# Kernel tuning notes

Measured on AMD Instinct MI355X. Metric: run time of the kernel, lower is better.

## Reference

```python
import jax, jax.numpy as jnp
import numpy as np

LN_EPS = 1e-5
NEG_INF = -1e30


def setup_inputs() -> dict:
    key = jax.random.key(0)
    ks = jax.random.split(key, 8)
    B, S, D_MODEL, Q_IN = 1, 2048, 1024, 512
    HI, DI = 16, 64            # indexer heads / head_dim
    H, DQK, DV = 8, 64, 64     # MLA heads, qk_head_dim, v_head_dim
    return {
        "x": jax.random.normal(ks[0], (B, S, D_MODEL), jnp.float32),
        "q_input": jax.random.normal(ks[1], (B, S, Q_IN), jnp.float32),
        "q": jax.random.normal(ks[2], (B, S, H, DQK), jnp.float32),
        "k": jax.random.normal(ks[3], (B, S, H, DQK), jnp.float32),
        "v": jax.random.normal(ks[4], (B, S, H, DV), jnp.float32),
        "w_q": jax.random.normal(ks[5], (Q_IN, HI * DI), jnp.float32) * (Q_IN ** -0.5),
        "w_k": jax.random.normal(ks[6], (D_MODEL, DI), jnp.float32) * (D_MODEL ** -0.5),
        "ln_g": jnp.ones((DI,), jnp.float32),
        "ln_b": jnp.zeros((DI,), jnp.float32),
        "w_weights": jax.random.normal(ks[7], (D_MODEL, HI), jnp.float32) * (D_MODEL ** -0.5),
        "top_k": 128,
    }


def _indexer_topk(x, q_input, w_q, w_k, ln_g, ln_b, w_weights, top_k):
    """Lightning indexer: per-head relevance scores -> weighted sum -> causal top-k indices."""
    B, S, _ = x.shape
    HI = w_weights.shape[1]
    DI = w_k.shape[1]
    qi = (q_input @ w_q).reshape(B, S, HI, DI)          # bqhd
    ki = x @ w_k                                         # bkd
    mu = ki.mean(-1, keepdims=True)
    var = ((ki - mu) ** 2).mean(-1, keepdims=True)
    ki = (ki - mu) * jax.lax.rsqrt(var + LN_EPS) * ln_g + ln_b
    # per-head weights; scores*w summed over h == (sum_h w*q) . k  (fused, same math)
    w = (x @ w_weights) * (HI ** -0.5)                   # bqh
    q_eff = jnp.einsum("bqhd,bqh->bqd", qi, w) * (DI ** -0.5)
    scores = jnp.einsum("bqd,bkd->bqk", q_eff, ki)       # [B,S,S]
    pos = jnp.arange(S)
    causal = jnp.where(pos[None, :] <= pos[:, None], 0.0, NEG_INF).astype(scores.dtype)
    scores = scores + causal[None]
    return jax.lax.top_k(scores, top_k)[1]               # [B,S,K]


def reference(x, q_input, q, k, v, w_q, w_k, ln_g, ln_b, w_weights, top_k):
    B, S, H, DQK = q.shape
    DV = v.shape[-1]
    idx = _indexer_topk(x, q_input, w_q, w_k, ln_g, ln_b, w_weights, top_k)  # [B,S,K]

    qh = q.transpose(0, 2, 1, 3)   # [B,H,Sq,D]
    kh = k.transpose(0, 2, 1, 3)   # [B,H,Sk,D]
    vh = v.transpose(0, 2, 1, 3)

    def gather(kv, ix):            # kv [Sk,D], ix [Sq,K] -> [Sq,K,D]
        return kv[ix]

    gather_h = jax.vmap(gather, in_axes=(0, None))       # over heads, shared idx
    gather_bh = jax.vmap(gather_h, in_axes=(0, 0))       # over batch
    k_sel = gather_bh(kh, idx)     # [B,H,Sq,K,D]
    v_sel = gather_bh(vh, idx)     # [B,H,Sq,K,Dv]

    att = jnp.einsum("bhqd,bhqkd->bhqk", qh, k_sel) * (DQK ** -0.5)
    pos = jnp.arange(S)
    valid = idx[:, None, :, :] <= pos[None, None, :, None]   # causal validity of gathered idx
    att = jnp.where(valid, att, NEG_INF)
    p = jax.nn.softmax(att, axis=-1)
    out = jnp.einsum("bhqk,bhqkd->bhqd", p, v_sel)
    return out.transpose(0, 2, 1, 3)   # [B,S,H,Dv]
```

## Files before the change

kernel.cpp:

```cpp
#include <hip/hip_runtime.h>
#include <hip/hip_bf16.h>
#include <hip/hip_fp16.h>
#include <math.h>

#define S 2048
#define DM 1024
#define QIN 512
#define HI 16
#define DI 64
#define NH 8
#define TOPK 128
#define LN_EPS 1e-5f
#define KP 8

typedef float f32x4 __attribute__((ext_vector_type(4)));
typedef short s16x8 __attribute__((ext_vector_type(8)));

__device__ __forceinline__ float wave_sum(float v){
#pragma unroll
  for (int o = 32; o; o >>= 1) v += __shfl_xor(v, o);
  return v;
}
__device__ __forceinline__ float wave_max(float v){
#pragma unroll
  for (int o = 32; o; o >>= 1) v = fmaxf(v, __shfl_xor(v, o));
  return v;
}
__device__ __forceinline__ unsigned short f2bf(float x){
  unsigned u = __float_as_uint(x);
  unsigned r = u + 0x7FFFu + ((u >> 16) & 1u);
  return (unsigned short)(r >> 16);
}
__device__ __forceinline__ float bf2f(unsigned short s){
  return __uint_as_float(((unsigned)s) << 16);
}
__device__ __forceinline__ unsigned short f2h(float x){
  return __half_as_ushort(__float2half_rn(x));
}
union UH2 { unsigned int u; __half2 h; };
__device__ __forceinline__ __half2 as_half2(unsigned int u){ UH2 x; x.u = u; return x.h; }

__global__ __launch_bounds__(256) void k_f1(const float* __restrict__ x,
                                            const float* __restrict__ wk,
                                            const float* __restrict__ ww,
                                            float* __restrict__ part,
                                            const float* __restrict__ qin,
                                            unsigned short* __restrict__ Ah,
                                            unsigned short* __restrict__ Al,
                                            const float* __restrict__ k,
                                            unsigned short* __restrict__ kh,
                                            const float* __restrict__ v,
                                            unsigned short* __restrict__ vh,
                                            const float* __restrict__ wq,
                                            unsigned short* __restrict__ Bh,
                                            unsigned short* __restrict__ Bl){
  __shared__ float As[32][68];
  __shared__ float Bs[32][84];
  const int bid = blockIdx.x;
  const int t = threadIdx.x;

  if (bid < 256){
    const int kp = bid & 7;
    const int bm = bid >> 3;
    const int m0 = bm * 64;
    const int tm = (t & 15) * 4;
    const int tn = (t >> 4) * 5;
    float acc[4][5];
#pragma unroll
    for (int i = 0; i < 4; i++)
#pragma unroll
      for (int j = 0; j < 5; j++) acc[i][j] = 0.f;

    for (int kb = 0; kb < (DM / KP) / 32; ++kb){
      const int k0 = kp * (DM / KP) + kb * 32;
#pragma unroll
      for (int i = 0; i < 2; i++){
        int u = t + i * 256;
        int m = u >> 3, c4 = u & 7;
        float4 a = *(const float4*)&x[(size_t)(m0 + m) * DM + k0 + c4 * 4];
        As[c4*4+0][m] = a.x; As[c4*4+1][m] = a.y; As[c4*4+2][m] = a.z; As[c4*4+3][m] = a.w;
      }
#pragma unroll
      for (int i = 0; i < 10; i++){
        int u = t + i * 256;
        int kk = u / 80, nn = u % 80;
        float val = (nn < 64) ? wk[(size_t)(k0 + kk) * 64 + nn]
                              : ww[(size_t)(k0 + kk) * 16 + (nn - 64)];
        Bs[kk][nn] = val;
      }
      __syncthreads();
#pragma unroll
      for (int kk = 0; kk < 32; ++kk){
        float4 a = *(const float4*)&As[kk][tm];
        float av[4] = {a.x, a.y, a.z, a.w};
        float bb[5];
#pragma unroll
        for (int j = 0; j < 5; j++) bb[j] = Bs[kk][tn + j];
#pragma unroll
        for (int i = 0; i < 4; i++)
#pragma unroll
          for (int j = 0; j < 5; j++) acc[i][j] = fmaf(av[i], bb[j], acc[i][j]);
      }
      __syncthreads();
    }
    float* dst = part + (size_t)kp * S * 80;
#pragma unroll
    for (int i = 0; i < 4; i++)
#pragma unroll
      for (int j = 0; j < 5; j++)
        dst[(size_t)(m0 + tm + i) * 80 + tn + j] = acc[i][j];
    return;
  }

  if (bid < 256 + 3072){
    const int SEG0 = S * QIN / 4;
    const int SEG1 = S * NH * 64 / 4;
    int id = (bid - 256) * 256 + t;
    if (id < SEG0){
      float4 f = ((const float4*)qin)[id];
      ushort4 h, lo;
      h.x = f2bf(f.x); lo.x = f2bf(f.x - bf2f(h.x));
      h.y = f2bf(f.y); lo.y = f2bf(f.y - bf2f(h.y));
      h.z = f2bf(f.z); lo.z = f2bf(f.z - bf2f(h.z));
      h.w = f2bf(f.w); lo.w = f2bf(f.w - bf2f(h.w));
      ((ushort4*)Ah)[id] = h;
      ((ushort4*)Al)[id] = lo;
    } else if (id < SEG0 + SEG1){
      int j = id - SEG0;
      float4 f = ((const float4*)k)[j];
      ushort4 o;
      o.x = f2h(f.x); o.y = f2h(f.y); o.z = f2h(f.z); o.w = f2h(f.w);
      ((ushort4*)kh)[j] = o;
    } else {
      int j = id - SEG0 - SEG1;
      float4 f = ((const float4*)v)[j];
      ushort4 o;
      o.x = f2h(f.x); o.y = f2h(f.y); o.z = f2h(f.z); o.w = f2h(f.w);
      ((ushort4*)vh)[j] = o;
    }
    return;
  }

  {
    unsigned short (*lh)[33] = (unsigned short(*)[33])&As[0][0];
    unsigned short (*ll)[33] = (unsigned short(*)[33])&Bs[0][0];
    const int b2 = bid - 3328;
    const int k0 = (b2 & 15) * 32;
    const int n0 = (b2 >> 4) * 32;
    const int c = t & 31, r8 = t >> 5;
#pragma unroll
    for (int i = 0; i < 4; ++i){
      int kk = r8 + i * 8;
      float wv = wq[(size_t)(k0 + kk) * 1024 + n0 + c];
      unsigned short h = f2bf(wv);
      lh[c][kk] = h;
      ll[c][kk] = f2bf(wv - bf2f(h));
    }
    __syncthreads();
    const int kk = t & 31, nl = t >> 5;
#pragma unroll
    for (int i = 0; i < 4; ++i){
      int nn = nl + i * 8;
      Bh[(size_t)(n0 + nn) * QIN + k0 + kk] = lh[nn][kk];
      Bl[(size_t)(n0 + nn) * QIN + k0 + kk] = ll[nn][kk];
    }
  }
}

__global__ __launch_bounds__(256) void k_f2(const float* __restrict__ part,
                                            const float* __restrict__ g,
                                            const float* __restrict__ b,
                                            float* __restrict__ ki,
                                            float* __restrict__ wgt,
                                            const unsigned short* __restrict__ Ah,
                                            const unsigned short* __restrict__ Al,
                                            const unsigned short* __restrict__ Bh,
                                            const unsigned short* __restrict__ Bl,
                                            float* __restrict__ qi){
  const int bid = blockIdx.x;
  if (bid < 512){
    const int s = bid * 4 + (threadIdx.x >> 6);
    const int l = threadIdx.x & 63;
    float kv = 0.f;
#pragma unroll
    for (int p = 0; p < KP; p++) kv += part[(size_t)p * S * 80 + (size_t)s * 80 + l];
    float wv = 0.f;
    if (l < 16){
#pragma unroll
      for (int p = 0; p < KP; p++) wv += part[(size_t)p * S * 80 + (size_t)s * 80 + 64 + l];
    }
    float mu = wave_sum(kv) * (1.f / 64.f);
    float d  = kv - mu;
    float var = wave_sum(d * d) * (1.f / 64.f);
    float o = d * (1.f / sqrtf(var + LN_EPS)) * g[l] + b[l];
    ki[(size_t)s * 64 + l] = o;
    if (l < 16) wgt[(size_t)s * 16 + l] = wv * 0.25f;
    return;
  }
  const int b2 = bid - 512;
  const int bn = b2 & 15;
  const int bm = b2 >> 4;
  const int w = threadIdx.x >> 6, l = threadIdx.x & 63;
  const int m0 = bm * 64 + (w >> 1) * 32;
  const int n0 = bn * 64 + (w & 1) * 32;
  const int r = l & 15, kg = l >> 4;

  f32x4 acc00 = {0,0,0,0}, acc01 = {0,0,0,0}, acc10 = {0,0,0,0}, acc11 = {0,0,0,0};

  const size_t aoff = (size_t)(m0 + r) * QIN + kg * 8;
  const size_t boff = (size_t)(n0 + r) * QIN + kg * 8;
#pragma unroll 4
  for (int k0 = 0; k0 < QIN; k0 += 32){
    s16x8 ah0 = *(const s16x8*)(Ah + aoff + k0);
    s16x8 ah1 = *(const s16x8*)(Ah + aoff + 16 * QIN + k0);
    s16x8 al0 = *(const s16x8*)(Al + aoff + k0);
    s16x8 al1 = *(const s16x8*)(Al + aoff + 16 * QIN + k0);
    s16x8 bh0 = *(const s16x8*)(Bh + boff + k0);
    s16x8 bh1 = *(const s16x8*)(Bh + boff + 16 * QIN + k0);
    s16x8 bl0 = *(const s16x8*)(Bl + boff + k0);
    s16x8 bl1 = *(const s16x8*)(Bl + boff + 16 * QIN + k0);
    acc00 = __builtin_amdgcn_mfma_f32_16x16x32_bf16(ah0, bh0, acc00, 0, 0, 0);
    acc00 = __builtin_amdgcn_mfma_f32_16x16x32_bf16(ah0, bl0, acc00, 0, 0, 0);
    acc00 = __builtin_amdgcn_mfma_f32_16x16x32_bf16(al0, bh0, acc00, 0, 0, 0);
    acc01 = __builtin_amdgcn_mfma_f32_16x16x32_bf16(ah0, bh1, acc01, 0, 0, 0);
    acc01 = __builtin_amdgcn_mfma_f32_16x16x32_bf16(ah0, bl1, acc01, 0, 0, 0);
    acc01 = __builtin_amdgcn_mfma_f32_16x16x32_bf16(al0, bh1, acc01, 0, 0, 0);
    acc10 = __builtin_amdgcn_mfma_f32_16x16x32_bf16(ah1, bh0, acc10, 0, 0, 0);
    acc10 = __builtin_amdgcn_mfma_f32_16x16x32_bf16(ah1, bl0, acc10, 0, 0, 0);
    acc10 = __builtin_amdgcn_mfma_f32_16x16x32_bf16(al1, bh0, acc10, 0, 0, 0);
    acc11 = __builtin_amdgcn_mfma_f32_16x16x32_bf16(ah1, bh1, acc11, 0, 0, 0);
    acc11 = __builtin_amdgcn_mfma_f32_16x16x32_bf16(ah1, bl1, acc11, 0, 0, 0);
    acc11 = __builtin_amdgcn_mfma_f32_16x16x32_bf16(al1, bh1, acc11, 0, 0, 0);
  }
#pragma unroll
  for (int j = 0; j < 4; ++j){
    qi[(size_t)(m0 +  0 + kg * 4 + j) * 1024 + n0 +  0 + r] = acc00[j];
    qi[(size_t)(m0 +  0 + kg * 4 + j) * 1024 + n0 + 16 + r] = acc01[j];
    qi[(size_t)(m0 + 16 + kg * 4 + j) * 1024 + n0 +  0 + r] = acc10[j];
    qi[(size_t)(m0 + 16 + kg * 4 + j) * 1024 + n0 + 16 + r] = acc11[j];
  }
}

__global__ __launch_bounds__(256) void k_qeff(const float* __restrict__ qi,
                                              const float* __restrict__ wgt,
                                              float* __restrict__ qe){
  const int id = blockIdx.x * 256 + threadIdx.x;
  const int s = id >> 6, d = id & 63;
  float acc = 0.f;
#pragma unroll
  for (int h = 0; h < 16; h++)
    acc = fmaf(wgt[(size_t)s * 16 + h], qi[(size_t)s * 1024 + h * 64 + d], acc);
  qe[(size_t)s * 64 + d] = acc * 0.125f;
}

__global__ __launch_bounds__(256) void k_scores(const float* __restrict__ qe,
                                                const float* __restrict__ ki,
                                                float* __restrict__ sc){
  const int bj = blockIdx.x, bi = blockIdx.y;
  if (bj > bi) return;
  const int t = threadIdx.x;
  const int i0 = bi * 64, j0 = bj * 64;
  __shared__ float Qs[64][68];
  __shared__ float Ks[64][68];
#pragma unroll
  for (int u0 = 0; u0 < 4; ++u0){
    int u = t + u0 * 256;
    int r = u >> 4, d4 = u & 15;
    float4 a = *(const float4*)&qe[(size_t)(i0 + r) * 64 + d4 * 4];
    Qs[d4*4+0][r] = a.x; Qs[d4*4+1][r] = a.y; Qs[d4*4+2][r] = a.z; Qs[d4*4+3][r] = a.w;
    float4 b = *(const float4*)&ki[(size_t)(j0 + r) * 64 + d4 * 4];
    Ks[d4*4+0][r] = b.x; Ks[d4*4+1][r] = b.y; Ks[d4*4+2][r] = b.z; Ks[d4*4+3][r] = b.w;
  }
  __syncthreads();
  const int tm = (t & 15) * 4, tn = (t >> 4) * 4;
  float acc[4][4] = {};
#pragma unroll
  for (int d = 0; d < 64; ++d){
    float4 a = *(const float4*)&Qs[d][tm];
    float4 b = *(const float4*)&Ks[d][tn];
    float av[4] = {a.x, a.y, a.z, a.w}, bb[4] = {b.x, b.y, b.z, b.w};
#pragma unroll
    for (int i = 0; i < 4; i++)
#pragma unroll
      for (int j = 0; j < 4; j++) acc[i][j] = fmaf(av[i], bb[j], acc[i][j]);
  }
#pragma unroll
  for (int i = 0; i < 4; i++)
#pragma unroll
    for (int j = 0; j < 4; j++)
      sc[(size_t)(i0 + tm + i) * S + j0 + tn + j] = acc[i][j];
}

__global__ __launch_bounds__(256) void k_topk(const float* __restrict__ sc,
                                              int* __restrict__ idx,
                                              int* __restrict__ cnt){
  const int i = blockIdx.x, t = threadIdx.x;
  const int w = t >> 6, l = t & 63;
  const int n = i + 1;
  int* outr = idx + (size_t)i * TOPK;
  if (n <= TOPK){
    for (int m = t; m < n; m += 256) outr[m] = m;
    if (t == 0) cnt[i] = n;
    return;
  }
  __shared__ unsigned int keys[S];
  __shared__ int lA[S];
  __shared__ int lB[S];
  __shared__ int hist[256];
  __shared__ int wtot[4];
  __shared__ int s_b, s_above, s_out, s_m;
  hist[t] = 0;
  if (t == 0) s_out = 0;
  __syncthreads();
  for (int j = t; j < n; j += 256){
    unsigned int u = __float_as_uint(sc[(size_t)i * S + j]);
    unsigned int kk = (u & 0x80000000u) ? ~u : (u | 0x80000000u);
    keys[j] = kk;
    atomicAdd(&hist[kk >> 24], 1);
  }
  __syncthreads();
  int rem = TOPK;
  {
    const int h = hist[t];
    int vsc = h;
#pragma unroll
    for (int off = 1; off < 64; off <<= 1){
      int u = __shfl_down(vsc, off);
      if (l + off < 64) vsc += u;
    }
    if (l == 0) wtot[w] = vsc;
    __syncthreads();
    int later = 0;
#pragma unroll
    for (int ww = 1; ww < 4; ++ww) if (ww > w) later += wtot[ww];
    const int excl = vsc + later - h;
    if (excl < rem && excl + h >= rem){ s_b = t; s_above = excl; }
    __syncthreads();
  }
  int b = s_b;
  rem -= s_above;
  if (t == 0) s_m = 0;
  __syncthreads();
  for (int j = t; j < n; j += 256){
    int by = keys[j] >> 24;
    if (by > b){ int p = atomicAdd(&s_out, 1); outr[p] = j; }
    else if (by == b){ int p = atomicAdd(&s_m, 1); lA[p] = j; }
  }
  __syncthreads();
  int m = s_m;
  int* Lsrc = lA; int* Ldst = lB;
  bool done = false;
  if (m == rem){
    int base = TOPK - rem;
    for (int u = t; u < m; u += 256) outr[base + u] = Lsrc[u];
    done = true;
  }
  for (int p = 2; p >= 0 && !done; --p){
    const int sh = p * 8;
    __syncthreads();
    hist[t] = 0;
    __syncthreads();
    for (int u = t; u < m; u += 256) atomicAdd(&hist[(keys[Lsrc[u]] >> sh) & 255], 1);
    __syncthreads();
    {
      const int h = hist[t];
      int vsc = h;
#pragma unroll
      for (int off = 1; off < 64; off <<= 1){
        int u = __shfl_down(vsc, off);
        if (l + off < 64) vsc += u;
      }
      if (l == 0) wtot[w] = vsc;
      __syncthreads();
// ... 82 lines not shown
    acc0 = __hfma2(as_half2(u0.y), qa2[1], acc0);
    acc0 = __hfma2(as_half2(u0.z), qa2[2], acc0);
    acc0 = __hfma2(as_half2(u0.w), qa2[3], acc0);
    acc1 = __hfma2(as_half2(u1.x), qb2[0], acc1);
    acc1 = __hfma2(as_half2(u1.y), qb2[1], acc1);
    acc1 = __hfma2(as_half2(u1.z), qb2[2], acc1);
    acc1 = __hfma2(as_half2(u1.w), qb2[3], acc1);
    float d0 = __low2float(acc0) + __high2float(acc0);
    float d1 = __low2float(acc1) + __high2float(acc1);
#pragma unroll
    for (int o = 1; o < 8; o <<= 1){ d0 += __shfl_xor(d0, o); d1 += __shfl_xor(d1, o); }
    if (gl == 0){ sp[w][0][j] = d0; sp[w][1][j] = d1; }
  }
  asm volatile("" ::: "memory");

  const bool v0 = (l < n), v1 = (l + 64 < n);
  {
    float s0 = v0 ? sp[w][0][l] : -1e30f, s1 = v1 ? sp[w][0][l + 64] : -1e30f;
    float m = wave_max(fmaxf(s0, s1));
    float e0 = v0 ? __expf(s0 - m) : 0.f;
    float e1 = v1 ? __expf(s1 - m) : 0.f;
    float inv = 1.f / wave_sum(e0 + e1);
    sp[w][0][l] = e0 * inv;
    sp[w][0][l + 64] = e1 * inv;
  }
  {
    float s0 = v0 ? sp[w][1][l] : -1e30f, s1 = v1 ? sp[w][1][l + 64] : -1e30f;
    float m = wave_max(fmaxf(s0, s1));
    float e0 = v0 ? __expf(s0 - m) : 0.f;
    float e1 = v1 ? __expf(s1 - m) : 0.f;
    float inv = 1.f / wave_sum(e0 + e1);
    sp[w][1][l] = e0 * inv;
    sp[w][1][l + 64] = e1 * inv;
  }
  asm volatile("" ::: "memory");

  const int kq = l >> 4;
  const int hp = (l >> 3) & 1;
  const int d8 = (l & 7) * 8;
  float o8[8] = {0,0,0,0,0,0,0,0};
#pragma unroll 4
  for (int pass = 0; pass < TOPK / 4; ++pass){
    const int j = pass * 4 + kq;
    const size_t base = (size_t)sidx[w][j] * (NH * 64);
    uint4 uv = *(const uint4*)(vh + base + (h0 + hp) * 64 + d8);
    float p = sp[w][hp][j];
    __half2 va = as_half2(uv.x), vb = as_half2(uv.y), vc = as_half2(uv.z), vd = as_half2(uv.w);
    o8[0] = fmaf(p, __low2float(va),  o8[0]);
    o8[1] = fmaf(p, __high2float(va), o8[1]);
    o8[2] = fmaf(p, __low2float(vb),  o8[2]);
    o8[3] = fmaf(p, __high2float(vb), o8[3]);
    o8[4] = fmaf(p, __low2float(vc),  o8[4]);
    o8[5] = fmaf(p, __high2float(vc), o8[5]);
    o8[6] = fmaf(p, __low2float(vd),  o8[6]);
    o8[7] = fmaf(p, __high2float(vd), o8[7]);
  }
#pragma unroll
  for (int e = 0; e < 8; ++e){
    o8[e] += __shfl_xor(o8[e], 16);
    o8[e] += __shfl_xor(o8[e], 32);
  }
  if (l < 16){
    float* dst = &out[(size_t)i * (NH * 64) + (h0 + hp) * 64 + d8];
    *(float4*)dst       = make_float4(o8[0], o8[1], o8[2], o8[3]);
    *(float4*)(dst + 4) = make_float4(o8[4], o8[5], o8[6], o8[7]);
  }
}

extern "C" void kernel_launch(void* const* d_in, const int* in_sizes, int n_in,
                              void* d_out, int out_size, void* d_ws, size_t ws_size,
                              hipStream_t stream){
  const float* x   = (const float*)d_in[0];
  const float* qin = (const float*)d_in[1];
  const float* q   = (const float*)d_in[2];
  const float* k   = (const float*)d_in[3];
  const float* v   = (const float*)d_in[4];
  const float* wq  = (const float*)d_in[5];
  const float* wk  = (const float*)d_in[6];
  const float* lng = (const float*)d_in[7];
  const float* lnb = (const float*)d_in[8];
  const float* ww  = (const float*)d_in[9];
  float* out = (float*)d_out;

  float* ws   = (float*)d_ws;
  float* part = ws;
  float* ki   = ws + 1310720;
  float* wgt  = ws + 1441792;
  float* qi   = ws + 1474560;
  float* qe   = ws + 3571712;
  float* sc   = ws + 3702784;
  int*   idx  = (int*)(ws + 7897088);
  int*   cnt  = (int*)(ws + 8159232);
  unsigned short* kh = (unsigned short*)(ws + 8161280);
  unsigned short* vh = kh + (size_t)S * NH * 64;
  unsigned short* Ah = (unsigned short*)sc;
  unsigned short* Al = Ah + (size_t)S * QIN;
  unsigned short* Bh = Al + (size_t)S * QIN;
  unsigned short* Bl = Bh + (size_t)1024 * QIN;

  hipLaunchKernelGGL(k_f1,     dim3(3840),   dim3(256), 0, stream,
                     x, wk, ww, part, qin, Ah, Al, k, kh, v, vh, wq, Bh, Bl);
  hipLaunchKernelGGL(k_f2,     dim3(1024),   dim3(256), 0, stream,
                     part, lng, lnb, ki, wgt, Ah, Al, Bh, Bl, qi);
  hipLaunchKernelGGL(k_qeff,   dim3(512),    dim3(256), 0, stream, qi, wgt, qe);
  hipLaunchKernelGGL(k_scores, dim3(32, 32), dim3(256), 0, stream, qe, ki, sc);
  hipLaunchKernelGGL(k_topk,   dim3(2048),   dim3(256), 0, stream, sc, idx, cnt);
  hipLaunchKernelGGL(k_attn,   dim3(2048),   dim3(256), 0, stream, q, kh, vh, idx, cnt, out);
}
```

Before: 113.7 us.

## Move x@w_k and indexer score GEMMs onto split-bf16 MFMA

Replaces the FP32 SIMT GEMM for x@w_k and the causal score GEMM with bf16 MFMA using a hi/lo split (three products) to keep near-FP32 accuracy. x and w_k are pre-split and transposed into bf16 buffers in the first kernel. The x@w_weights product becomes a naive per-thread dot product, and the q_eff and layernorm steps are fused into a new k_f3 that emits split bf16 operands. The cost is extra conversion traffic for x (two 4MB bf16 copies) and a naive weights GEMV, traded for far fewer FP32 FMA cycles in the matmuls.

```diff
diff --git a/kernel.cpp b/kernel.cpp
--- a/kernel.cpp
+++ b/kernel.cpp
@@ -11,7 +11,6 @@
 #define NH 8
 #define TOPK 128
 #define LN_EPS 1e-5f
-#define KP 8
 
 typedef float f32x4 __attribute__((ext_vector_type(4)));
 typedef short s16x8 __attribute__((ext_vector_type(8)));
@@ -40,111 +39,43 @@
 union UH2 { unsigned int u; __half2 h; };
 __device__ __forceinline__ __half2 as_half2(unsigned int u){ UH2 x; x.u = u; return x.h; }
 
+
 __global__ __launch_bounds__(256) void k_f1(const float* __restrict__ x,
+                                            const float* __restrict__ ww,
+                                            float* __restrict__ wgt,
+                                            const float* __restrict__ wq,
+                                            unsigned short* __restrict__ Bh,
+                                            unsigned short* __restrict__ Bl,
                                             const float* __restrict__ wk,
-                                            const float* __restrict__ ww,
-                                            float* __restrict__ part,
+                                            unsigned short* __restrict__ Wh,
+                                            unsigned short* __restrict__ Wl,
+                                            unsigned short* __restrict__ Xh,
+                                            unsigned short* __restrict__ Xl,
                                             const float* __restrict__ qin,
                                             unsigned short* __restrict__ Ah,
                                             unsigned short* __restrict__ Al,
                                             const float* __restrict__ k,
                                             unsigned short* __restrict__ kh,
                                             const float* __restrict__ v,
-                                            unsigned short* __restrict__ vh,
-                                            const float* __restrict__ wq,
-                                            unsigned short* __restrict__ Bh,
-                                            unsigned short* __restrict__ Bl){
-  __shared__ float As[32][68];
-  __shared__ float Bs[32][84];
+                                            unsigned short* __restrict__ vh){
+  __shared__ unsigned short lh[32][33];
+  __shared__ unsigned short ll[32][33];
   const int bid = blockIdx.x;
   const int t = threadIdx.x;
 
-  if (bid < 256){
-    const int kp = bid & 7;
-    const int bm = bid >> 3;
-    const int m0 = bm * 64;
-    const int tm = (t & 15) * 4;
-    const int tn = (t >> 4) * 5;
-    float acc[4][5];
-#pragma unroll
-    for (int i = 0; i < 4; i++)
-#pragma unroll
-      for (int j = 0; j < 5; j++) acc[i][j] = 0.f;
-
-    for (int kb = 0; kb < (DM / KP) / 32; ++kb){
-      const int k0 = kp * (DM / KP) + kb * 32;
-#pragma unroll
-      for (int i = 0; i < 2; i++){
-        int u = t + i * 256;
-        int m = u >> 3, c4 = u & 7;
-        float4 a = *(const float4*)&x[(size_t)(m0 + m) * DM + k0 + c4 * 4];
-        As[c4*4+0][m] = a.x; As[c4*4+1][m] = a.y; As[c4*4+2][m] = a.z; As[c4*4+3][m] = a.w;
-      }
-#pragma unroll
-      for (int i = 0; i < 10; i++){
-        int u = t + i * 256;
-        int kk = u / 80, nn = u % 80;
-        float val = (nn < 64) ? wk[(size_t)(k0 + kk) * 64 + nn]
-                              : ww[(size_t)(k0 + kk) * 16 + (nn - 64)];
-        Bs[kk][nn] = val;
-      }
-      __syncthreads();
-#pragma unroll
-      for (int kk = 0; kk < 32; ++kk){
-        float4 a = *(const float4*)&As[kk][tm];
-        float av[4] = {a.x, a.y, a.z, a.w};
-        float bb[5];
-#pragma unroll
-        for (int j = 0; j < 5; j++) bb[j] = Bs[kk][tn + j];
-#pragma unroll
-        for (int i = 0; i < 4; i++)
-#pragma unroll
-          for (int j = 0; j < 5; j++) acc[i][j] = fmaf(av[i], bb[j], acc[i][j]);
-      }
-      __syncthreads();
-    }
-    float* dst = part + (size_t)kp * S * 80;
-#pragma unroll
-    for (int i = 0; i < 4; i++)
-#pragma unroll
-      for (int j = 0; j < 5; j++)
-        dst[(size_t)(m0 + tm + i) * 80 + tn + j] = acc[i][j];
-    return;
-  }
-
-  if (bid < 256 + 3072){
-    const int SEG0 = S * QIN / 4;
-    const int SEG1 = S * NH * 64 / 4;
-    int id = (bid - 256) * 256 + t;
-    if (id < SEG0){
-      float4 f = ((const float4*)qin)[id];
-      ushort4 h, lo;
-      h.x = f2bf(f.x); lo.x = f2bf(f.x - bf2f(h.x));
-      h.y = f2bf(f.y); lo.y = f2bf(f.y - bf2f(h.y));
-      h.z = f2bf(f.z); lo.z = f2bf(f.z - bf2f(h.z));
-      h.w = f2bf(f.w); lo.w = f2bf(f.w - bf2f(h.w));
-      ((ushort4*)Ah)[id] = h;
-      ((ushort4*)Al)[id] = lo;
-    } else if (id < SEG0 + SEG1){
-      int j = id - SEG0;
-      float4 f = ((const float4*)k)[j];
-      ushort4 o;
-      o.x = f2h(f.x); o.y = f2h(f.y); o.z = f2h(f.z); o.w = f2h(f.w);
-      ((ushort4*)kh)[j] = o;
-    } else {
-      int j = id - SEG0 - SEG1;
-      float4 f = ((const float4*)v)[j];
-      ushort4 o;
-      o.x = f2h(f.x); o.y = f2h(f.y); o.z = f2h(f.z); o.w = f2h(f.w);
-      ((ushort4*)vh)[j] = o;
-    }
-    return;
-  }
-
-  {
-    unsigned short (*lh)[33] = (unsigned short(*)[33])&As[0][0];
-    unsigned short (*ll)[33] = (unsigned short(*)[33])&Bs[0][0];
-    const int b2 = bid - 3328;
+  if (bid < 128){
+    const int row = bid * 16 + (t >> 4);
+    const int col = t & 15;
+    const float* xr = x + (size_t)row * DM;
+    float acc = 0.f;
+#pragma unroll 8
+    for (int kk = 0; kk < DM; ++kk)
+      acc = fmaf(xr[kk], ww[(size_t)kk * HI + col], acc);
+    wgt[(size_t)row * HI + col] = acc * 0.25f;
+    return;
+  }
+  if (bid < 640){
+    const int b2 = bid - 128;
     const int k0 = (b2 & 15) * 32;
     const int n0 = (b2 >> 4) * 32;
     const int c = t & 31, r8 = t >> 5;
@@ -164,49 +95,134 @@
       Bh[(size_t)(n0 + nn) * QIN + k0 + kk] = lh[nn][kk];
       Bl[(size_t)(n0 + nn) * QIN + k0 + kk] = ll[nn][kk];
     }
-  }
-}
-
-__global__ __launch_bounds__(256) void k_f2(const float* __restrict__ part,
-                                            const float* __restrict__ g,
-                                            const float* __restrict__ b,
-                                            float* __restrict__ ki,
-                                            float* __restrict__ wgt,
+    return;
+  }
+  if (bid < 704){
+    const int b2 = bid - 640;
+    const int k0 = (b2 & 31) * 32;
+    const int n0 = (b2 >> 5) * 32;
+    const int c = t & 31, r8 = t >> 5;
+#pragma unroll
+    for (int i = 0; i < 4; ++i){
+      int kk = r8 + i * 8;
+      float wv = wk[(size_t)(k0 + kk) * 64 + n0 + c];
+      unsigned short h = f2bf(wv);
+      lh[c][kk] = h;
+      ll[c][kk] = f2bf(wv - bf2f(h));
+    }
+    __syncthreads();
+    const int kk = t & 31, nl = t >> 5;
+#pragma unroll
+    for (int i = 0; i < 4; ++i){
+      int nn = nl + i * 8;
+      Wh[(size_t)(n0 + nn) * DM + k0 + kk] = lh[nn][kk];
+      Wl[(size_t)(n0 + nn) * DM + k0 + kk] = ll[nn][kk];
+    }
+    return;
+  }
+  if (bid < 2752){
+    int id = (bid - 704) * 256 + t;
+    float4 f = ((const float4*)x)[id];
+    ushort4 h, lo;
+    h.x = f2bf(f.x); lo.x = f2bf(f.x - bf2f(h.x));
+    h.y = f2bf(f.y); lo.y = f2bf(f.y - bf2f(h.y));
+    h.z = f2bf(f.z); lo.z = f2bf(f.z - bf2f(h.z));
+    h.w = f2bf(f.w); lo.w = f2bf(f.w - bf2f(h.w));
+    ((ushort4*)Xh)[id] = h;
+    ((ushort4*)Xl)[id] = lo;
+    return;
+  }
+  if (bid < 3776){
+    int id = (bid - 2752) * 256 + t;
+    float4 f = ((const float4*)qin)[id];
+    ushort4 h, lo;
+    h.x = f2bf(f.x); lo.x = f2bf(f.x - bf2f(h.x));
+    h.y = f2bf(f.y); lo.y = f2bf(f.y - bf2f(h.y));
+    h.z = f2bf(f.z); lo.z = f2bf(f.z - bf2f(h.z));
+    h.w = f2bf(f.w); lo.w = f2bf(f.w - bf2f(h.w));
+    ((ushort4*)Ah)[id] = h;
+    ((ushort4*)Al)[id] = lo;
+    return;
+  }
+  if (bid < 4800){
+    int id = (bid - 3776) * 256 + t;
+    float4 f = ((const float4*)k)[id];
+    ushort4 o;
+    o.x = f2h(f.x); o.y = f2h(f.y); o.z = f2h(f.z); o.w = f2h(f.w);
+    ((ushort4*)kh)[id] = o;
+    return;
+  }
+  {
+    int id = (bid - 4800) * 256 + t;
+    float4 f = ((const float4*)v)[id];
+    ushort4 o;
+    o.x = f2h(f.x); o.y = f2h(f.y); o.z = f2h(f.z); o.w = f2h(f.w);
+    ((ushort4*)vh)[id] = o;
+  }
+}
+
+__global__ __launch_bounds__(256) void k_f2(const unsigned short* __restrict__ Xh,
+                                            const unsigned short* __restrict__ Xl,
+                                            const unsigned short* __restrict__ Wh,
+                                            const unsigned short* __restrict__ Wl,
+                                            float* __restrict__ part,
                                             const unsigned short* __restrict__ Ah,
                                             const unsigned short* __restrict__ Al,
                                             const unsigned short* __restrict__ Bh,
                                             const unsigned short* __restrict__ Bl,
                                             float* __restrict__ qi){
   const int bid = blockIdx.x;
-  if (bid < 512){
-    const int s = bid * 4 + (threadIdx.x >> 6);
-    const int l = threadIdx.x & 63;
-    float kv = 0.f;
-#pragma unroll
-    for (int p = 0; p < KP; p++) kv += part[(size_t)p * S * 80 + (size_t)s * 80 + l];
-    float wv = 0.f;
-    if (l < 16){
-#pragma unroll
-      for (int p = 0; p < KP; p++) wv += part[(size_t)p * S * 80 + (size_t)s * 80 + 64 + l];
-    }
-    float mu = wave_sum(kv) * (1.f / 64.f);
-    float d  = kv - mu;
-    float var = wave_sum(d * d) * (1.f / 64.f);
-    float o = d * (1.f / sqrtf(var + LN_EPS)) * g[l] + b[l];
-    ki[(size_t)s * 64 + l] = o;
-    if (l < 16) wgt[(size_t)s * 16 + l] = wv * 0.25f;
-    return;
-  }
-  const int b2 = bid - 512;
+  const int w = threadIdx.x >> 6, l = threadIdx.x & 63;
+  const int r = l & 15, kg = l >> 4;
+
+  if (bid < 128){
+    const int kp = bid & 3;
+    const int bm = bid >> 2;
+    const int m0 = bm * 64 + (w >> 1) * 32;
+    const int n0 = (w & 1) * 32;
+    const int kbase = kp * 256;
+    f32x4 acc00 = {0,0,0,0}, acc01 = {0,0,0,0}, acc10 = {0,0,0,0}, acc11 = {0,0,0,0};
+    const size_t aoff = (size_t)(m0 + r) * DM + kbase + kg * 8;
+    const size_t boff = (size_t)(n0 + r) * DM + kbase + kg * 8;
+#pragma unroll 4
+    for (int k0 = 0; k0 < 256; k0 += 32){
+      s16x8 ah0 = *(const s16x8*)(Xh + aoff + k0);
+      s16x8 ah1 = *(const s16x8*)(Xh + aoff + 16 * DM + k0);
+      s16x8 al0 = *(const s16x8*)(Xl + aoff + k0);
+      s16x8 al1 = *(const s16x8*)(Xl + aoff + 16 * DM + k0);
+      s16x8 bh0 = *(const s16x8*)(Wh + boff + k0);
+      s16x8 bh1 = *(const s16x8*)(Wh + boff + 16 * DM + k0);
+      s16x8 bl0 = *(const s16x8*)(Wl + boff + k0);
+      s16x8 bl1 = *(const s16x8*)(Wl + boff + 16 * DM + k0);
+      acc00 = __builtin_amdgcn_mfma_f32_16x16x32_bf16(ah0, bh0, acc00, 0, 0, 0);
+      acc00 = __builtin_amdgcn_mfma_f32_16x16x32_bf16(ah0, bl0, acc00, 0, 0, 0);
+      acc00 = __builtin_amdgcn_mfma_f32_16x16x32_bf16(al0, bh0, acc00, 0, 0, 0);
+      acc01 = __builtin_amdgcn_mfma_f32_16x16x32_bf16(ah0, bh1, acc01, 0, 0, 0);
+      acc01 = __builtin_amdgcn_mfma_f32_16x16x32_bf16(ah0, bl1, acc01, 0, 0, 0);
+      acc01 = __builtin_amdgcn_mfma_f32_16x16x32_bf16(al0, bh1, acc01, 0, 0, 0);
+      acc10 = __builtin_amdgcn_mfma_f32_16x16x32_bf16(ah1, bh0, acc10, 0, 0, 0);
+      acc10 = __builtin_amdgcn_mfma_f32_16x16x32_bf16(ah1, bl0, acc10, 0, 0, 0);
+      acc10 = __builtin_amdgcn_mfma_f32_16x16x32_bf16(al1, bh0, acc10, 0, 0, 0);
+      acc11 = __builtin_amdgcn_mfma_f32_16x16x32_bf16(ah1, bh1, acc11, 0, 0, 0);
+      acc11 = __builtin_amdgcn_mfma_f32_16x16x32_bf16(ah1, bl1, acc11, 0, 0, 0);
+      acc11 = __builtin_amdgcn_mfma_f32_16x16x32_bf16(al1, bh1, acc11, 0, 0, 0);
+    }
+    float* dst = part + (size_t)kp * S * 64;
+#pragma unroll
+    for (int j = 0; j < 4; ++j){
+      dst[(size_t)(m0 +  0 + kg * 4 + j) * 64 + n0 +  0 + r] = acc00[j];
+      dst[(size_t)(m0 +  0 + kg * 4 + j) * 64 + n0 + 16 + r] = acc01[j];
+      dst[(size_t)(m0 + 16 + kg * 4 + j) * 64 + n0 +  0 + r] = acc10[j];
+      dst[(size_t)(m0 + 16 + kg * 4 + j) * 64 + n0 + 16 + r] = acc11[j];
+    }
+    return;
+  }
+  const int b2 = bid - 128;
   const int bn = b2 & 15;
   const int bm = b2 >> 4;
-  const int w = threadIdx.x >> 6, l = threadIdx.x & 63;
   const int m0 = bm * 64 + (w >> 1) * 32;
   const int n0 = bn * 64 + (w & 1) * 32;
-  const int r = l & 15, kg = l >> 4;
-
   f32x4 acc00 = {0,0,0,0}, acc01 = {0,0,0,0}, acc10 = {0,0,0,0}, acc11 = {0,0,0,0};
-
   const size_t aoff = (size_t)(m0 + r) * QIN + kg * 8;
   const size_t boff = (size_t)(n0 + r) * QIN + kg * 8;
 #pragma unroll 4
@@ -241,54 +257,87 @@
   }
 }
 
-__global__ __launch_bounds__(256) void k_qeff(const float* __restrict__ qi,
-                                              const float* __restrict__ wgt,
-                                              float* __restrict__ qe){
-  const int id = blockIdx.x * 256 + threadIdx.x;
+__global__ __launch_bounds__(256) void k_f3(const float* __restrict__ part,
+                                            const float* __restrict__ g,
+                                            const float* __restrict__ b,
+                                            unsigned short* __restrict__ kih,
+                                            unsigned short* __restrict__ kil,
+                                            const float* __restrict__ qi,
+                                            const float* __restrict__ wgt,
+                                            unsigned short* __restrict__ qeh,
+                                            unsigned short* __restrict__ qel){
+  const int bid = blockIdx.x;
+  if (bid < 512){
+    const int s = bid * 4 + (threadIdx.x >> 6);
+    const int l = threadIdx.x & 63;
+    float kv = 0.f;
+#pragma unroll
+    for (int p = 0; p < 4; p++) kv += part[(size_t)p * S * 64 + (size_t)s * 64 + l];
+    float mu = wave_sum(kv) * (1.f / 64.f);
+    float d  = kv - mu;
+    float var = wave_sum(d * d) * (1.f / 64.f);
+    float o = d * (1.f / sqrtf(var + LN_EPS)) * g[l] + b[l];
+    unsigned short h = f2bf(o);
+    kih[(size_t)s * 64 + l] = h;
+    kil[(size_t)s * 64 + l] = f2bf(o - bf2f(h));
+    return;
+  }
+  const int id = (bid - 512) * 256 + threadIdx.x;
   const int s = id >> 6, d = id & 63;
   float acc = 0.f;
 #pragma unroll
   for (int h = 0; h < 16; h++)
     acc = fmaf(wgt[(size_t)s * 16 + h], qi[(size_t)s * 1024 + h * 64 + d], acc);
-  qe[(size_t)s * 64 + d] = acc * 0.125f;
-}
-
-__global__ __launch_bounds__(256) void k_scores(const float* __restrict__ qe,
-                                                const float* __restrict__ ki,
+  acc *= 0.125f;
+  unsigned short hh = f2bf(acc);
+  qeh[(size_t)s * 64 + d] = hh;
+  qel[(size_t)s * 64 + d] = f2bf(acc - bf2f(hh));
+}
+
+__global__ __launch_bounds__(256) void k_scores(const unsigned short* __restrict__ qeh,
+                                                const unsigned short* __restrict__ qel,
+                                                const unsigned short* __restrict__ kih,
+                                                const unsigned short* __restrict__ kil,
                                                 float* __restrict__ sc){
   const int bj = blockIdx.x, bi = blockIdx.y;
   if (bj > bi) return;
-  const int t = threadIdx.x;
-  const int i0 = bi * 64, j0 = bj * 64;
-  __shared__ float Qs[64][68];
-  __shared__ float Ks[64][68];
-#pragma unroll
-  for (int u0 = 0; u0 < 4; ++u0){
-    int u = t + u0 * 256;
-    int r = u >> 4, d4 = u & 15;
-    float4 a = *(const float4*)&qe[(size_t)(i0 + r) * 64 + d4 * 4];
-    Qs[d4*4+0][r] = a.x; Qs[d4*4+1][r] = a.y; Qs[d4*4+2][r] = a.z; Qs[d4*4+3][r] = a.w;
-    float4 b = *(const float4*)&ki[(size_t)(j0 + r) * 64 + d4 * 4];
-    Ks[d4*4+0][r] = b.x; Ks[d4*4+1][r] = b.y; Ks[d4*4+2][r] = b.z; Ks[d4*4+3][r] = b.w;
-  }
-  __syncthreads();
-  const int tm = (t & 15) * 4, tn = (t >> 4) * 4;
-  float acc[4][4] = {};
-#pragma unroll
-  for (int d = 0; d < 64; ++d){
-    float4 a = *(const float4*)&Qs[d][tm];
-    float4 b = *(const float4*)&Ks[d][tn];
-    float av[4] = {a.x, a.y, a.z, a.w}, bb[4] = {b.x, b.y, b.z, b.w};
-#pragma unroll
-    for (int i = 0; i < 4; i++)
-#pragma unroll
-      for (int j = 0; j < 4; j++) acc[i][j] = fmaf(av[i], bb[j], acc[i][j]);
-  }
-#pragma unroll
-  for (int i = 0; i < 4; i++)
-#pragma unroll
-    for (int j = 0; j < 4; j++)
-      sc[(size_t)(i0 + tm + i) * S + j0 + tn + j] = acc[i][j];
+  const int w = threadIdx.x >> 6, l = threadIdx.x & 63;
+  const int r = l & 15, kg = l >> 4;
+  const int m0 = bi * 64 + (w >> 1) * 32;
+  const int n0 = bj * 64 + (w & 1) * 32;
+  f32x4 acc00 = {0,0,0,0}, acc01 = {0,0,0,0}, acc10 = {0,0,0,0}, acc11 = {0,0,0,0};
+  const size_t aoff = (size_t)(m0 + r) * 64 + kg * 8;
+  const size_t boff = (size_t)(n0 + r) * 64 + kg * 8;
+#pragma unroll
+  for (int k0 = 0; k0 < 64; k0 += 32){
+    s16x8 ah0 = *(const s16x8*)(qeh + aoff + k0);
+    s16x8 ah1 = *(const s16x8*)(qeh + aoff + 16 * 64 + k0);
+    s16x8 al0 = *(const s16x8*)(qel + aoff + k0);
+    s16x8 al1 = *(const s16x8*)(qel + aoff + 16 * 64 + k0);
+    s16x8 bh0 = *(const s16x8*)(kih + boff + k0);
+    s16x8 bh1 = *(const s16x8*)(kih + boff + 16 * 64 + k0);
+    s16x8 bl0 = *(const s16x8*)(kil + boff + k0);
+    s16x8 bl1 = *(const s16x8*)(kil + boff + 16 * 64 + k0);
+    acc00 = __builtin_amdgcn_mfma_f32_16x16x32_bf16(ah0, bh0, acc00, 0, 0, 0);
+    acc00 = __builtin_amdgcn_mfma_f32_16x16x32_bf16(ah0, bl0, acc00, 0, 0, 0);
+    acc00 = __builtin_amdgcn_mfma_f32_16x16x32_bf16(al0, bh0, acc00, 0, 0, 0);
+    acc01 = __builtin_amdgcn_mfma_f32_16x16x32_bf16(ah0, bh1, acc01, 0, 0, 0);
+    acc01 = __builtin_amdgcn_mfma_f32_16x16x32_bf16(ah0, bl1, acc01, 0, 0, 0);
+    acc01 = __builtin_amdgcn_mfma_f32_16x16x32_bf16(al0, bh1, acc01, 0, 0, 0);
+    acc10 = __builtin_amdgcn_mfma_f32_16x16x32_bf16(ah1, bh0, acc10, 0, 0, 0);
+    acc10 = __builtin_amdgcn_mfma_f32_16x16x32_bf16(ah1, bl0, acc10, 0, 0, 0);
+    acc10 = __builtin_amdgcn_mfma_f32_16x16x32_bf16(al1, bh0, acc10, 0, 0, 0);
+    acc11 = __builtin_amdgcn_mfma_f32_16x16x32_bf16(ah1, bh1, acc11, 0, 0, 0);
+    acc11 = __builtin_amdgcn_mfma_f32_16x16x32_bf16(ah1, bl1, acc11, 0, 0, 0);
+    acc11 = __builtin_amdgcn_mfma_f32_16x16x32_bf16(al1, bh1, acc11, 0, 0, 0);
+  }
+#pragma unroll
+  for (int j = 0; j < 4; ++j){
+    sc[(size_t)(m0 +  0 + kg * 4 + j) * S + n0 +  0 + r] = acc00[j];
+    sc[(size_t)(m0 +  0 + kg * 4 + j) * S + n0 + 16 + r] = acc01[j];
+    sc[(size_t)(m0 + 16 + kg * 4 + j) * S + n0 +  0 + r] = acc10[j];
+    sc[(size_t)(m0 + 16 + kg * 4 + j) * S + n0 + 16 + r] = acc11[j];
+  }
 }
 
 __global__ __launch_bounds__(256) void k_topk(const float* __restrict__ sc,
@@ -539,26 +588,33 @@
 
   float* ws   = (float*)d_ws;
   float* part = ws;
-  float* ki   = ws + 1310720;
-  float* wgt  = ws + 1441792;
-  float* qi   = ws + 1474560;
-  float* qe   = ws + 3571712;
-  float* sc   = ws + 3702784;
-  int*   idx  = (int*)(ws + 7897088);
-  int*   cnt  = (int*)(ws + 8159232);
-  unsigned short* kh = (unsigned short*)(ws + 8161280);
-  unsigned short* vh = kh + (size_t)S * NH * 64;
+  float* wgt  = ws + 524288;
+  float* qi   = ws + 557056;
+  float* sc   = ws + 2654208;
+  int*   idx  = (int*)(ws + 6848512);
+  int*   cnt  = (int*)(ws + 7110656);
+  unsigned short* kh  = (unsigned short*)(ws + 7112704);
+  unsigned short* vh  = (unsigned short*)(ws + 7636992);
+  unsigned short* kih = (unsigned short*)(ws + 8161280);
+  unsigned short* kil = (unsigned short*)(ws + 8226816);
+  unsigned short* qeh = (unsigned short*)(ws + 8292352);
+  unsigned short* qel = (unsigned short*)(ws + 8357888);
   unsigned short* Ah = (unsigned short*)sc;
   unsigned short* Al = Ah + (size_t)S * QIN;
   unsigned short* Bh = Al + (size_t)S * QIN;
   unsigned short* Bl = Bh + (size_t)1024 * QIN;
-
-  hipLaunchKernelGGL(k_f1,     dim3(3840),   dim3(256), 0, stream,
-                     x, wk, ww, part, qin, Ah, Al, k, kh, v, vh, wq, Bh, Bl);
-  hipLaunchKernelGGL(k_f2,     dim3(1024),   dim3(256), 0, stream,
-                     part, lng, lnb, ki, wgt, Ah, Al, Bh, Bl, qi);
-  hipLaunchKernelGGL(k_qeff,   dim3(512),    dim3(256), 0, stream, qi, wgt, qe);
-  hipLaunchKernelGGL(k_scores, dim3(32, 32), dim3(256), 0, stream, qe, ki, sc);
+  unsigned short* Xh = Bl + (size_t)1024 * QIN;
+  unsigned short* Xl = Xh + (size_t)S * DM;
+  unsigned short* Wh = Xl + (size_t)S * DM;
+  unsigned short* Wl = Wh + (size_t)64 * DM;
+
+  hipLaunchKernelGGL(k_f1,     dim3(5824),   dim3(256), 0, stream,
+                     x, ww, wgt, wq, Bh, Bl, wk, Wh, Wl, Xh, Xl, qin, Ah, Al, k, kh, v, vh);
+  hipLaunchKernelGGL(k_f2,     dim3(640),    dim3(256), 0, stream,
+                     Xh, Xl, Wh, Wl, part, Ah, Al, Bh, Bl, qi);
+  hipLaunchKernelGGL(k_f3,     dim3(1024),   dim3(256), 0, stream,
+                     part, lng, lnb, kih, kil, qi, wgt, qeh, qel);
+  hipLaunchKernelGGL(k_scores, dim3(32, 32), dim3(256), 0, stream, qeh, qel, kih, kil, sc);
   hipLaunchKernelGGL(k_topk,   dim3(2048),   dim3(256), 0, stream, sc, idx, cnt);
   hipLaunchKernelGGL(k_attn,   dim3(2048),   dim3(256), 0, stream, q, kh, vh, idx, cnt, out);
 }
```

Result: slower. 137.8 us (+21.2%).

## Compute indexer scores with split-bf16 MFMA and split-K the q projection

Applied to the files above, without the earlier changes.

The FP32 FMA score GEMM (qe·ki^T) becomes a six-pass bf16x3 split MFMA GEMM. To feed it, qe and ki are emitted as hi/mid/lo bf16 triples. The q_input@w_q GEMM is split in two along K to double the block count, and k_qeff is replaced by k_f3, which sums the two partials. The workspace layout is redone so the split operands no longer alias the scores buffer. The cost is extra partial-sum traffic and six MFMA passes, and the split precision could flip near-tie top-k choices.

```diff
diff --git a/kernel.cpp b/kernel.cpp
--- a/kernel.cpp
+++ b/kernel.cpp
@@ -39,6 +39,19 @@
 }
 union UH2 { unsigned int u; __half2 h; };
 __device__ __forceinline__ __half2 as_half2(unsigned int u){ UH2 x; x.u = u; return x.h; }
+
+#define MFMA3(ACC, AH, AL, BH, BL) \
+  ACC = __builtin_amdgcn_mfma_f32_16x16x32_bf16(AH, BH, ACC, 0, 0, 0); \
+  ACC = __builtin_amdgcn_mfma_f32_16x16x32_bf16(AH, BL, ACC, 0, 0, 0); \
+  ACC = __builtin_amdgcn_mfma_f32_16x16x32_bf16(AL, BH, ACC, 0, 0, 0);
+
+#define MFMA6(ACC, AH, AM, AL, BH, BM, BL) \
+  ACC = __builtin_amdgcn_mfma_f32_16x16x32_bf16(AH, BH, ACC, 0, 0, 0); \
+  ACC = __builtin_amdgcn_mfma_f32_16x16x32_bf16(AH, BM, ACC, 0, 0, 0); \
+  ACC = __builtin_amdgcn_mfma_f32_16x16x32_bf16(AM, BH, ACC, 0, 0, 0); \
+  ACC = __builtin_amdgcn_mfma_f32_16x16x32_bf16(AH, BL, ACC, 0, 0, 0); \
+  ACC = __builtin_amdgcn_mfma_f32_16x16x32_bf16(AL, BH, ACC, 0, 0, 0); \
+  ACC = __builtin_amdgcn_mfma_f32_16x16x32_bf16(AM, BM, ACC, 0, 0, 0);
 
 __global__ __launch_bounds__(256) void k_f1(const float* __restrict__ x,
                                             const float* __restrict__ wk,
@@ -170,7 +183,9 @@
 __global__ __launch_bounds__(256) void k_f2(const float* __restrict__ part,
                                             const float* __restrict__ g,
                                             const float* __restrict__ b,
-                                            float* __restrict__ ki,
+                                            unsigned short* __restrict__ kih,
+                                            unsigned short* __restrict__ kim,
+                                            unsigned short* __restrict__ kil,
                                             float* __restrict__ wgt,
                                             const unsigned short* __restrict__ Ah,
                                             const unsigned short* __restrict__ Al,
@@ -193,24 +208,30 @@
     float d  = kv - mu;
     float var = wave_sum(d * d) * (1.f / 64.f);
     float o = d * (1.f / sqrtf(var + LN_EPS)) * g[l] + b[l];
-    ki[(size_t)s * 64 + l] = o;
+    unsigned short h = f2bf(o);
+    float r1 = o - bf2f(h);
+    unsigned short m = f2bf(r1);
+    kih[(size_t)s * 64 + l] = h;
+    kim[(size_t)s * 64 + l] = m;
+    kil[(size_t)s * 64 + l] = f2bf(r1 - bf2f(m));
     if (l < 16) wgt[(size_t)s * 16 + l] = wv * 0.25f;
     return;
   }
   const int b2 = bid - 512;
-  const int bn = b2 & 15;
-  const int bm = b2 >> 4;
+  const int kp = b2 & 1;
+  const int bidx = b2 >> 1;
+  const int bn = bidx & 15;
+  const int bm = bidx >> 4;
   const int w = threadIdx.x >> 6, l = threadIdx.x & 63;
+  const int r = l & 15, kg = l >> 4;
   const int m0 = bm * 64 + (w >> 1) * 32;
   const int n0 = bn * 64 + (w & 1) * 32;
-  const int r = l & 15, kg = l >> 4;
-
+  const int kbase = kp * 256;
   f32x4 acc00 = {0,0,0,0}, acc01 = {0,0,0,0}, acc10 = {0,0,0,0}, acc11 = {0,0,0,0};
-
-  const size_t aoff = (size_t)(m0 + r) * QIN + kg * 8;
-  const size_t boff = (size_t)(n0 + r) * QIN + kg * 8;
+  const size_t aoff = (size_t)(m0 + r) * QIN + kbase + kg * 8;
+  const size_t boff = (size_t)(n0 + r) * QIN + kbase + kg * 8;
 #pragma unroll 4
-  for (int k0 = 0; k0 < QIN; k0 += 32){
+  for (int k0 = 0; k0 < 256; k0 += 32){
     s16x8 ah0 = *(const s16x8*)(Ah + aoff + k0);
     s16x8 ah1 = *(const s16x8*)(Ah + aoff + 16 * QIN + k0);
     s16x8 al0 = *(const s16x8*)(Al + aoff + k0);
@@ -219,76 +240,87 @@
     s16x8 bh1 = *(const s16x8*)(Bh + boff + 16 * QIN + k0);
     s16x8 bl0 = *(const s16x8*)(Bl + boff + k0);
     s16x8 bl1 = *(const s16x8*)(Bl + boff + 16 * QIN + k0);
-    acc00 = __builtin_amdgcn_mfma_f32_16x16x32_bf16(ah0, bh0, acc00, 0, 0, 0);
-    acc00 = __builtin_amdgcn_mfma_f32_16x16x32_bf16(ah0, bl0, acc00, 0, 0, 0);
-    acc00 = __builtin_amdgcn_mfma_f32_16x16x32_bf16(al0, bh0, acc00, 0, 0, 0);
-    acc01 = __builtin_amdgcn_mfma_f32_16x16x32_bf16(ah0, bh1, acc01, 0, 0, 0);
-    acc01 = __builtin_amdgcn_mfma_f32_16x16x32_bf16(ah0, bl1, acc01, 0, 0, 0);
-    acc01 = __builtin_amdgcn_mfma_f32_16x16x32_bf16(al0, bh1, acc01, 0, 0, 0);
-    acc10 = __builtin_amdgcn_mfma_f32_16x16x32_bf16(ah1, bh0, acc10, 0, 0, 0);
-    acc10 = __builtin_amdgcn_mfma_f32_16x16x32_bf16(ah1, bl0, acc10, 0, 0, 0);
-    acc10 = __builtin_amdgcn_mfma_f32_16x16x32_bf16(al1, bh0, acc10, 0, 0, 0);
-    acc11 = __builtin_amdgcn_mfma_f32_16x16x32_bf16(ah1, bh1, acc11, 0, 0, 0);
-    acc11 = __builtin_amdgcn_mfma_f32_16x16x32_bf16(ah1, bl1, acc11, 0, 0, 0);
-    acc11 = __builtin_amdgcn_mfma_f32_16x16x32_bf16(al1, bh1, acc11, 0, 0, 0);
-  }
+    MFMA3(acc00, ah0, al0, bh0, bl0)
+    MFMA3(acc01, ah0, al0, bh1, bl1)
+    MFMA3(acc10, ah1, al1, bh0, bl0)
+    MFMA3(acc11, ah1, al1, bh1, bl1)
+  }
+  float* qip = qi + (size_t)kp * S * 1024;
 #pragma unroll
   for (int j = 0; j < 4; ++j){
-    qi[(size_t)(m0 +  0 + kg * 4 + j) * 1024 + n0 +  0 + r] = acc00[j];
-    qi[(size_t)(m0 +  0 + kg * 4 + j) * 1024 + n0 + 16 + r] = acc01[j];
-    qi[(size_t)(m0 + 16 + kg * 4 + j) * 1024 + n0 +  0 + r] = acc10[j];
-    qi[(size_t)(m0 + 16 + kg * 4 + j) * 1024 + n0 + 16 + r] = acc11[j];
-  }
-}
-
-__global__ __launch_bounds__(256) void k_qeff(const float* __restrict__ qi,
-                                              const float* __restrict__ wgt,
-                                              float* __restrict__ qe){
+    qip[(size_t)(m0 +  0 + kg * 4 + j) * 1024 + n0 +  0 + r] = acc00[j];
+    qip[(size_t)(m0 +  0 + kg * 4 + j) * 1024 + n0 + 16 + r] = acc01[j];
+    qip[(size_t)(m0 + 16 + kg * 4 + j) * 1024 + n0 +  0 + r] = acc10[j];
+    qip[(size_t)(m0 + 16 + kg * 4 + j) * 1024 + n0 + 16 + r] = acc11[j];
+  }
+}
+
+__global__ __launch_bounds__(256) void k_f3(const float* __restrict__ qi,
+                                            const float* __restrict__ wgt,
+                                            unsigned short* __restrict__ qeh,
+                                            unsigned short* __restrict__ qem,
+                                            unsigned short* __restrict__ qel){
   const int id = blockIdx.x * 256 + threadIdx.x;
   const int s = id >> 6, d = id & 63;
+  const float* qiA = qi;
+  const float* qiB = qi + (size_t)S * 1024;
   float acc = 0.f;
 #pragma unroll
-  for (int h = 0; h < 16; h++)
-    acc = fmaf(wgt[(size_t)s * 16 + h], qi[(size_t)s * 1024 + h * 64 + d], acc);
-  qe[(size_t)s * 64 + d] = acc * 0.125f;
-}
-
-__global__ __launch_bounds__(256) void k_scores(const float* __restrict__ qe,
-                                                const float* __restrict__ ki,
+  for (int h = 0; h < 16; h++){
+    float qv = qiA[(size_t)s * 1024 + h * 64 + d] + qiB[(size_t)s * 1024 + h * 64 + d];
+    acc = fmaf(wgt[(size_t)s * 16 + h], qv, acc);
+  }
+  acc *= 0.125f;
+  unsigned short hh = f2bf(acc);
+  float r1 = acc - bf2f(hh);
+  unsigned short mm = f2bf(r1);
+  qeh[(size_t)s * 64 + d] = hh;
+  qem[(size_t)s * 64 + d] = mm;
+  qel[(size_t)s * 64 + d] = f2bf(r1 - bf2f(mm));
+}
+
+__global__ __launch_bounds__(256) void k_scores(const unsigned short* __restrict__ qeh,
+                                                const unsigned short* __restrict__ qem,
+                                                const unsigned short* __restrict__ qel,
+                                                const unsigned short* __restrict__ kih,
+                                                const unsigned short* __restrict__ kim,
+                                                const unsigned short* __restrict__ kil,
                                                 float* __restrict__ sc){
   const int bj = blockIdx.x, bi = blockIdx.y;
   if (bj > bi) return;
-  const int t = threadIdx.x;
-  const int i0 = bi * 64, j0 = bj * 64;
-  __shared__ float Qs[64][68];
-  __shared__ float Ks[64][68];
-#pragma unroll
-  for (int u0 = 0; u0 < 4; ++u0){
-    int u = t + u0 * 256;
-    int r = u >> 4, d4 = u & 15;
-    float4 a = *(const float4*)&qe[(size_t)(i0 + r) * 64 + d4 * 4];
-    Qs[d4*4+0][r] = a.x; Qs[d4*4+1][r] = a.y; Qs[d4*4+2][r] = a.z; Qs[d4*4+3][r] = a.w;
-    float4 b = *(const float4*)&ki[(size_t)(j0 + r) * 64 + d4 * 4];
-    Ks[d4*4+0][r] = b.x; Ks[d4*4+1][r] = b.y; Ks[d4*4+2][r] = b.z; Ks[d4*4+3][r] = b.w;
-  }
-  __syncthreads();
-  const int tm = (t & 15) * 4, tn = (t >> 4) * 4;
-  float acc[4][4] = {};
-#pragma unroll
-  for (int d = 0; d < 64; ++d){
-    float4 a = *(const float4*)&Qs[d][tm];
-    float4 b = *(const float4*)&Ks[d][tn];
-    float av[4] = {a.x, a.y, a.z, a.w}, bb[4] = {b.x, b.y, b.z, b.w};
-#pragma unroll
-    for (int i = 0; i < 4; i++)
-#pragma unroll
-      for (int j = 0; j < 4; j++) acc[i][j] = fmaf(av[i], bb[j], acc[i][j]);
-  }
-#pragma unroll
-  for (int i = 0; i < 4; i++)
-#pragma unroll
-    for (int j = 0; j < 4; j++)
-      sc[(size_t)(i0 + tm + i) * S + j0 + tn + j] = acc[i][j];
+  const int w = threadIdx.x >> 6, l = threadIdx.x & 63;
+  const int r = l & 15, kg = l >> 4;
+  const int m0 = bi * 64 + (w >> 1) * 32;
+  const int n0 = bj * 64 + (w & 1) * 32;
+  f32x4 acc00 = {0,0,0,0}, acc01 = {0,0,0,0}, acc10 = {0,0,0,0}, acc11 = {0,0,0,0};
+  const size_t aoff = (size_t)(m0 + r) * 64 + kg * 8;
+  const size_t boff = (size_t)(n0 + r) * 64 + kg * 8;
+#pragma unroll
+  for (int k0 = 0; k0 < 64; k0 += 32){
+    s16x8 ah0 = *(const s16x8*)(qeh + aoff + k0);
+    s16x8 ah1 = *(const s16x8*)(qeh + aoff + 16 * 64 + k0);
+    s16x8 am0 = *(const s16x8*)(qem + aoff + k0);
+    s16x8 am1 = *(const s16x8*)(qem + aoff + 16 * 64 + k0);
+    s16x8 al0 = *(const s16x8*)(qel + aoff + k0);
+    s16x8 al1 = *(const s16x8*)(qel + aoff + 16 * 64 + k0);
+    s16x8 bh0 = *(const s16x8*)(kih + boff + k0);
+    s16x8 bh1 = *(const s16x8*)(kih + boff + 16 * 64 + k0);
+    s16x8 bm0 = *(const s16x8*)(kim + boff + k0);
+    s16x8 bm1 = *(const s16x8*)(kim + boff + 16 * 64 + k0);
+    s16x8 bl0 = *(const s16x8*)(kil + boff + k0);
+    s16x8 bl1 = *(const s16x8*)(kil + boff + 16 * 64 + k0);
+    MFMA6(acc00, ah0, am0, al0, bh0, bm0, bl0)
+    MFMA6(acc01, ah0, am0, al0, bh1, bm1, bl1)
+    MFMA6(acc10, ah1, am1, al1, bh0, bm0, bl0)
+    MFMA6(acc11, ah1, am1, al1, bh1, bm1, bl1)
+  }
+#pragma unroll
+  for (int j = 0; j < 4; ++j){
+    sc[(size_t)(m0 +  0 + kg * 4 + j) * S + n0 +  0 + r] = acc00[j];
+    sc[(size_t)(m0 +  0 + kg * 4 + j) * S + n0 + 16 + r] = acc01[j];
+    sc[(size_t)(m0 + 16 + kg * 4 + j) * S + n0 +  0 + r] = acc10[j];
+    sc[(size_t)(m0 + 16 + kg * 4 + j) * S + n0 + 16 + r] = acc11[j];
+  }
 }
 
 __global__ __launch_bounds__(256) void k_topk(const float* __restrict__ sc,
@@ -537,28 +569,34 @@
   const float* ww  = (const float*)d_in[9];
   float* out = (float*)d_out;
 
-  float* ws   = (float*)d_ws;
+  float* ws = (float*)d_ws;
   float* part = ws;
-  float* ki   = ws + 1310720;
-  float* wgt  = ws + 1441792;
-  float* qi   = ws + 1474560;
-  float* qe   = ws + 3571712;
-  float* sc   = ws + 3702784;
-  int*   idx  = (int*)(ws + 7897088);
-  int*   cnt  = (int*)(ws + 8159232);
-  unsigned short* kh = (unsigned short*)(ws + 8161280);
-  unsigned short* vh = kh + (size_t)S * NH * 64;
-  unsigned short* Ah = (unsigned short*)sc;
-  unsigned short* Al = Ah + (size_t)S * QIN;
-  unsigned short* Bh = Al + (size_t)S * QIN;
-  unsigned short* Bl = Bh + (size_t)1024 * QIN;
+  float* wgt  = ws + 1310720;
+  float* qi   = ws + 1343488;
+  float* sc   = ws + 5537792;
+  int*   idx  = (int*)(ws + 9732096);
+  int*   cnt  = (int*)(ws + 9994240);
+  unsigned short* kh  = (unsigned short*)(ws + 9996288);
+  unsigned short* vh  = (unsigned short*)(ws + 10520576);
+  unsigned short* kih = (unsigned short*)(ws + 11044864);
+  unsigned short* kim = (unsigned short*)(ws + 11110400);
+  unsigned short* kil = (unsigned short*)(ws + 11175936);
+  unsigned short* qeh = (unsigned short*)(ws + 11241472);
+  unsigned short* qem = (unsigned short*)(ws + 11307008);
+  unsigned short* qel = (unsigned short*)(ws + 11372544);
+  unsigned short* Ah  = (unsigned short*)(ws + 11438080);
+  unsigned short* Al  = (unsigned short*)(ws + 11962368);
+  unsigned short* Bh  = (unsigned short*)(ws + 12486656);
+  unsigned short* Bl  = (unsigned short*)(ws + 12748800);
 
   hipLaunchKernelGGL(k_f1,     dim3(3840),   dim3(256), 0, stream,
                      x, wk, ww, part, qin, Ah, Al, k, kh, v, vh, wq, Bh, Bl);
-  hipLaunchKernelGGL(k_f2,     dim3(1024),   dim3(256), 0, stream,
-                     part, lng, lnb, ki, wgt, Ah, Al, Bh, Bl, qi);
-  hipLaunchKernelGGL(k_qeff,   dim3(512),    dim3(256), 0, stream, qi, wgt, qe);
-  hipLaunchKernelGGL(k_scores, dim3(32, 32), dim3(256), 0, stream, qe, ki, sc);
+  hipLaunchKernelGGL(k_f2,     dim3(1536),   dim3(256), 0, stream,
+                     part, lng, lnb, kih, kim, kil, wgt, Ah, Al, Bh, Bl, qi);
+  hipLaunchKernelGGL(k_f3,     dim3(512),    dim3(256), 0, stream,
+                     qi, wgt, qeh, qem, qel);
+  hipLaunchKernelGGL(k_scores, dim3(32, 32), dim3(256), 0, stream,
+                     qeh, qem, qel, kih, kim, kil, sc);
   hipLaunchKernelGGL(k_topk,   dim3(2048),   dim3(256), 0, stream, sc, idx, cnt);
   hipLaunchKernelGGL(k_attn,   dim3(2048),   dim3(256), 0, stream, q, kh, vh, idx, cnt, out);
 }
```

Result: slower. 118.1 us, median of 2 (+3.9%).
